# Performance work log

Hardware: AMD Instinct MI355X
Metric: run time of the kernel (lower is better)

Reference implementation:

```python
import jax, jax.numpy as jnp
import numpy as np

B, H, W, C = 16, 192, 192, 128   # batch, height, width, d_inner
R = 16      # lora_rank (bottleneck width between lora_down and lora_up)
RK = 8      # internal LoRA rank = lora_rank // 2
NC = 5      # cache_size
SCALE = 1.0 / RK        # alpha / rank with alpha = 1.0
THRESH = 0.7            # similarity_threshold
EPS = 1e-8              # torch cosine_similarity eps


def _lora_paths(x, A1, B1, A2, B2):
    # lora_down: C -> RK -> R, lora_up: R -> RK -> C, each scaled by 1/RK (dropout off in eval)
    down = ((x @ A1) @ B1) * SCALE          # [B,H,W,R]
    up = ((down @ A2) @ B2) * SCALE         # [B,H,W,C]
    return down, up


def setup_inputs() -> dict:
    key = jax.random.key(0)
    ks = jax.random.split(key, 9)
    x = jax.random.normal(ks[0], (B, H, W, C), dtype=jnp.float32)
    A1 = (jax.random.normal(ks[1], (C, RK)) / np.sqrt(C)).astype(jnp.float32)
    B1 = (jax.random.normal(ks[2], (RK, R)) / np.sqrt(RK)).astype(jnp.float32)
    A2 = (jax.random.normal(ks[3], (R, RK)) / np.sqrt(R)).astype(jnp.float32)
    B2 = (jax.random.normal(ks[4], (RK, C)) / np.sqrt(RK)).astype(jnp.float32)
    W1 = (jax.random.normal(ks[5], (C + R, C)) / np.sqrt(C + R)).astype(jnp.float32)
    b1 = jnp.zeros((C,), dtype=jnp.float32)
    W2 = (jax.random.normal(ks[6], (C, C)) / np.sqrt(C)).astype(jnp.float32)
    b2 = jnp.zeros((C,), dtype=jnp.float32)
    cache_w = jnp.array(0.5, dtype=jnp.float32)
    # Build cache entries as noisy copies of x_lora[:NC] so the first NC batch
    # elements clear the 0.7 cosine threshold (fused branch) and the rest do not.
    _, xl = _lora_paths(x, A1, B1, A2, B2)
    noise = jax.random.normal(ks[7], (NC, H, W, C), dtype=jnp.float32) * (0.05 * jnp.std(xl))
    cache_feats = xl[:NC] + noise           # [NC,H,W,C]
    return {"x": x, "A1": A1, "B1": B1, "A2": A2, "B2": B2,
            "W1": W1, "b1": b1, "W2": W2, "b2": b2,
            "cache_w": cache_w, "cache_feats": cache_feats}


def reference(x, A1, B1, A2, B2, W1, b1, W2, b2, cache_w, cache_feats):
    down, x_lora = _lora_paths(x, A1, B1, A2, B2)   # [B,H,W,R], [B,H,W,C]
    # Per-channel cosine similarity over the HW axis, averaged over channels
    num = jnp.einsum('bhwc,nhwc->bnc', x_lora, cache_feats)        # [B,NC,C]
    xn = jnp.sqrt(jnp.sum(x_lora * x_lora, axis=(1, 2)))           # [B,C]
    cn = jnp.sqrt(jnp.sum(cache_feats * cache_feats, axis=(1, 2))) # [NC,C]
    denom = jnp.maximum(xn[:, None, :], EPS) * jnp.maximum(cn[None, :, :], EPS)
    sims = jnp.mean(num / denom, axis=-1)                          # [B,NC]
    best_idx = jnp.argmax(sims, axis=1)                            # first max, like list.index
    best_sim = jnp.max(sims, axis=1)
    best = cache_feats[best_idx]                                   # [B,H,W,C]
    # Gated blend with cached feature, then fusion MLP on concat([blend, lora_down])
    cw = jax.nn.sigmoid(cache_w)
    blend = cw * x_lora + (1.0 - cw) * best
    h = jnp.concatenate([blend, down], axis=-1) @ W1 + b1          # [B,H,W,C]
    fused = jax.nn.silu(h) @ W2 + b2
    mask = (best_sim > THRESH)[:, None, None, None]
    return jnp.where(mask, fused, x_lora)
```

## Files before the change

kernel.cpp:

```cpp
#include <hip/hip_runtime.h>
#include <math.h>

#define BATCH 16
#define HWPIX 36864
#define CCH 128
#define NCACHE 5
#define SCALE 0.125f
#define THRESH 0.7f
#define EPSV 1e-8f

typedef _Float16 f16;
typedef __attribute__((ext_vector_type(8))) _Float16 f16x8;
typedef __attribute__((ext_vector_type(4))) float f32x4;

__global__ __launch_bounds__(256) void kpre1(
    const float* __restrict__ A1, const float* __restrict__ B1,
    const float* __restrict__ A2, const float* __restrict__ B2,
    const float* __restrict__ W1, const float* __restrict__ W2,
    const float* __restrict__ cache_w,
    float* __restrict__ M1f, float* __restrict__ M12f,
    f16* __restrict__ M12h, f16* __restrict__ Qh, f16* __restrict__ W2h) {
  __shared__ float M1s[128 * 16];
  __shared__ float M2s[16 * 128];
  int t = threadIdx.x;
  for (int idx = t; idx < 2048; idx += 256) {
    int i = idx >> 4, r = idx & 15;
    float s = 0.f;
    for (int k = 0; k < 8; ++k) s += A1[i * 8 + k] * B1[k * 16 + r];
    s *= SCALE;
    M1s[idx] = s;
    M1f[idx] = s;
  }
  for (int idx = t; idx < 2048; idx += 256) {
    int r = idx >> 7, j = idx & 127;
    float s = 0.f;
    for (int k = 0; k < 8; ++k) s += A2[r * 8 + k] * B2[k * 128 + j];
    M2s[idx] = s * SCALE;
  }
  __syncthreads();
  for (int idx = t; idx < 16384; idx += 256) {
    int i = idx >> 7, j = idx & 127;
    float s = 0.f;
    for (int r = 0; r < 16; ++r) s += M1s[i * 16 + r] * M2s[r * 128 + j];
    M12f[idx] = s;
    M12h[(((i >> 3) * 128 + j) << 3) + (i & 7)] = (f16)s;
  }
  float cw = 1.f / (1.f + __expf(-cache_w[0]));
  float qs = 1.f - cw;
  for (int idx = t; idx < 16384; idx += 256) {
    int k = idx >> 7, n = idx & 127;
    int ci = (((k >> 3) * 128 + n) << 3) + (k & 7);
    Qh[ci] = (f16)(qs * W1[k * 128 + n]);
    W2h[ci] = (f16)W2[k * 128 + n];
  }
}

__global__ __launch_bounds__(256) void kpre2(
    const float* __restrict__ W1, const float* __restrict__ M1f,
    const float* __restrict__ M12f, const float* __restrict__ cache_w,
    f16* __restrict__ Ph) {
  int t = threadIdx.x;
  int k = blockIdx.x * 8 + (t >> 5);
  int n0 = (t & 31) * 4;
  float cw = 1.f / (1.f + __expf(-cache_w[0]));
  float sa[4] = {0, 0, 0, 0}, sb[4] = {0, 0, 0, 0};
  for (int tt = 0; tt < 128; ++tt) {
    float m = M12f[k * 128 + tt];
    const float* wr = &W1[tt * 128 + n0];
    sa[0] += m * wr[0]; sa[1] += m * wr[1]; sa[2] += m * wr[2]; sa[3] += m * wr[3];
  }
  for (int r = 0; r < 16; ++r) {
    float m = M1f[k * 16 + r];
    const float* wr = &W1[(128 + r) * 128 + n0];
    sb[0] += m * wr[0]; sb[1] += m * wr[1]; sb[2] += m * wr[2]; sb[3] += m * wr[3];
  }
  for (int u = 0; u < 4; ++u) {
    int n = n0 + u;
    Ph[(((k >> 3) * 128 + n) << 3) + (k & 7)] = (f16)(cw * sa[u] + sb[u]);
  }
}

__global__ __launch_bounds__(256) void k2(
    const float* __restrict__ x, const float* __restrict__ cache,
    const f16* __restrict__ M12h, float* __restrict__ out,
    float* __restrict__ num, float* __restrict__ xn2, float* __restrict__ cn2) {
  __shared__ f16 Bs[16 * 128 * 8];
  __shared__ f16 As[16 * 64 * 8];
  __shared__ f16 XLb[64 * 132];
  __shared__ float nacc[2][5][128];
  __shared__ float x2acc[2][128];
  int t = threadIdx.x;
  int chunk = blockIdx.x;
  int grp = blockIdx.y;
  long pb = (long)chunk * 64;
  {
    const uint4* src = (const uint4*)M12h;
    uint4* dst = (uint4*)Bs;
    for (int i = t; i < 2048; i += 256) dst[i] = src[i];
  }
  int lane = t & 63, w = t >> 6, l15 = lane & 15, q = lane >> 4;
  for (int g = 0; g < 8; ++g) {
    int b = grp * 8 + g;
    const float* xb = x + ((long)b * HWPIX + pb) * CCH;
    __syncthreads();
    for (int i = 0; i < 8; ++i) {
      int f = i * 256 + t;
      int p = f >> 5, c4 = (f & 31) << 2;
      float4 v = ((const float4*)xb)[f];
      f16* d = &As[(((c4 >> 3) * 64 + p) << 3) + (c4 & 7)];
      d[0] = (f16)v.x; d[1] = (f16)v.y; d[2] = (f16)v.z; d[3] = (f16)v.w;
    }
    __syncthreads();
    f32x4 acc[8];
    for (int ni = 0; ni < 8; ++ni) acc[ni] = 0;
    for (int kk = 0; kk < 4; ++kk) {
      f16x8 a = *(const f16x8*)&As[(((kk * 4 + q) * 64 + (w * 16 + l15)) << 3)];
      for (int ni = 0; ni < 8; ++ni) {
        f16x8 bb = *(const f16x8*)&Bs[(((kk * 4 + q) * 128 + ni * 16 + l15)) << 3];
        acc[ni] = __builtin_amdgcn_mfma_f32_16x16x32_f16(a, bb, acc[ni], 0, 0, 0);
      }
    }
    float* ob = out + ((long)b * HWPIX + pb) * CCH;
    for (int ni = 0; ni < 8; ++ni) {
      int c = ni * 16 + l15;
      for (int r = 0; r < 4; ++r) {
        int p = w * 16 + q * 4 + r;
        float v = acc[ni][r];
        ob[(long)p * CCH + c] = v;
        XLb[p * 132 + c] = (f16)v;
      }
    }
    __syncthreads();
    {
      int c = t & 127, half = t >> 7;
      bool docn = (grp == 0) && (g == 0);
      float s2 = 0, sn0 = 0, sn1 = 0, sn2 = 0, sn3 = 0, sn4 = 0;
      float sc0 = 0, sc1 = 0, sc2 = 0, sc3 = 0, sc4 = 0;
      const float* cb = cache + pb * CCH + c;
      for (int pp = 0; pp < 32; ++pp) {
        int p = half * 32 + pp;
        float xl = (float)XLb[p * 132 + c];
        s2 += xl * xl;
        float cv0 = cb[((long)0 * HWPIX + p) * CCH];
        float cv1 = cb[((long)1 * HWPIX + p) * CCH];
        float cv2 = cb[((long)2 * HWPIX + p) * CCH];
        float cv3 = cb[((long)3 * HWPIX + p) * CCH];
        float cv4 = cb[((long)4 * HWPIX + p) * CCH];
        sn0 += xl * cv0; sn1 += xl * cv1; sn2 += xl * cv2;
        sn3 += xl * cv3; sn4 += xl * cv4;
        if (docn) {
          sc0 += cv0 * cv0; sc1 += cv1 * cv1; sc2 += cv2 * cv2;
          sc3 += cv3 * cv3; sc4 += cv4 * cv4;
        }
      }
      nacc[half][0][c] = sn0; nacc[half][1][c] = sn1; nacc[half][2][c] = sn2;
      nacc[half][3][c] = sn3; nacc[half][4][c] = sn4;
      x2acc[half][c] = s2;
      if (docn) {
        atomicAdd(&cn2[0 * 128 + c], sc0);
        atomicAdd(&cn2[1 * 128 + c], sc1);
        atomicAdd(&cn2[2 * 128 + c], sc2);
        atomicAdd(&cn2[3 * 128 + c], sc3);
        atomicAdd(&cn2[4 * 128 + c], sc4);
      }
    }
    __syncthreads();
    for (int idx = t; idx < 640; idx += 256) {
      int n = idx >> 7, cc = idx & 127;
      atomicAdd(&num[((long)b * 5 + n) * 128 + cc],
                nacc[0][n][cc] + nacc[1][n][cc]);
    }
    if (t < 128) atomicAdd(&xn2[b * 128 + t], x2acc[0][t] + x2acc[1][t]);
  }
}

__global__ __launch_bounds__(128) void k3(
    const float* __restrict__ num, const float* __restrict__ xn2v,
    const float* __restrict__ cn2v, int* __restrict__ stats) {
  __shared__ float sims[16][5];
  int t = threadIdx.x;
  if (t < 80) {
    int b = t / 5, n = t % 5;
    float s = 0.f;
    for (int c = 0; c < 128; ++c) {
      float xn = sqrtf(xn2v[b * 128 + c]);
      float cn = sqrtf(cn2v[n * 128 + c]);
      s += num[(b * 5 + n) * 128 + c] / (fmaxf(xn, EPSV) * fmaxf(cn, EPSV));
    }
    sims[b][n] = s * (1.f / 128.f);
  }
  __syncthreads();
  if (t < 16) {
    float bv = -1e30f;
    int bi = 0;
    for (int n = 0; n < 5; ++n) {
      float v = sims[t][n];
      if (v > bv) { bv = v; bi = n; }
    }
    stats[t] = bi;
    stats[16 + t] = (bv > THRESH) ? 1 : 0;
  }
}

__global__ __launch_bounds__(256) void k4(
    const float* __restrict__ x, const float* __restrict__ cache,
    const f16* __restrict__ Ph, const f16* __restrict__ Qh,
    const f16* __restrict__ W2h, const float* __restrict__ b1,
    const float* __restrict__ b2, const int* __restrict__ stats,
    float* __restrict__ out) {
  int b = blockIdx.y;
  if (!stats[16 + b]) return;
  __shared__ f16 Bs[16 * 128 * 8];
  __shared__ f16 As[16 * 64 * 8];
  __shared__ float b1s[128], b2s[128];
  int t = threadIdx.x;
  if (t < 128) { b1s[t] = b1[t]; b2s[t] = b2[t]; }
  int bi = stats[b];
  long pb = (long)blockIdx.x * 64;
  const float* xb = x + ((long)b * HWPIX + pb) * CCH;
  const float* cbest = cache + ((long)bi * HWPIX + pb) * CCH;
  int lane = t & 63, w = t >> 6, l15 = lane & 15, q = lane >> 4;

  auto stageA = [&](const float* __restrict__ src) {
    for (int i = 0; i < 8; ++i) {
      int f = i * 256 + t;
      int p = f >> 5, c4 = (f & 31) << 2;
      float4 v = ((const float4*)src)[f];
      f16* d = &As[(((c4 >> 3) * 64 + p) << 3) + (c4 & 7)];
      d[0] = (f16)v.x; d[1] = (f16)v.y; d[2] = (f16)v.z; d[3] = (f16)v.w;
    }
  };
  auto loadB = [&](const f16* __restrict__ src) {
    const uint4* s = (const uint4*)src;
    uint4* d = (uint4*)Bs;
    for (int i = t; i < 2048; i += 256) d[i] = s[i];
  };
  auto gemm = [&](f32x4* ac) {
    for (int kk = 0; kk < 4; ++kk) {
      f16x8 a = *(const f16x8*)&As[(((kk * 4 + q) * 64 + (w * 16 + l15)) << 3)];
      for (int ni = 0; ni < 8; ++ni) {
        f16x8 bb = *(const f16x8*)&Bs[(((kk * 4 + q) * 128 + ni * 16 + l15)) << 3];
        ac[ni] = __builtin_amdgcn_mfma_f32_16x16x32_f16(a, bb, ac[ni], 0, 0, 0);
      }
    }
  };

  f32x4 acc[8];
  for (int ni = 0; ni < 8; ++ni) acc[ni] = 0;
  loadB(Ph);
  stageA(xb);
  __syncthreads();
  gemm(acc);
  __syncthreads();
  loadB(Qh);
  stageA(cbest);
  __syncthreads();
  gemm(acc);
  for (int ni = 0; ni < 8; ++ni) {
    int c = ni * 16 + l15;
    for (int r = 0; r < 4; ++r) {
      int p = w * 16 + q * 4 + r;
      float hv = acc[ni][r] + b1s[c];
      float sv = hv / (1.f + __expf(-hv));
      As[(((c >> 3) * 64 + p) << 3) + (c & 7)] = (f16)sv;
    }
  }
  __syncthreads();
  loadB(W2h);
  __syncthreads();
  f32x4 acc2[8];
  for (int ni = 0; ni < 8; ++ni) acc2[ni] = 0;
  gemm(acc2);
  float* ob = out + ((long)b * HWPIX + pb) * CCH;
  for (int ni = 0; ni < 8; ++ni) {
    int c = ni * 16 + l15;
    for (int r = 0; r < 4; ++r) {
      int p = w * 16 + q * 4 + r;
      ob[(long)p * CCH + c] = acc2[ni][r] + b2s[c];
    }
  }
}

extern "C" void kernel_launch(void* const* d_in, const int* in_sizes, int n_in,
                              void* d_out, int out_size, void* d_ws, size_t ws_size,
                              hipStream_t stream) {
  const float* x  = (const float*)d_in[0];
  const float* A1 = (const float*)d_in[1];
  const float* B1 = (const float*)d_in[2];
  const float* A2 = (const float*)d_in[3];
  const float* B2 = (const float*)d_in[4];
  const float* W1 = (const float*)d_in[5];
  const float* b1 = (const float*)d_in[6];
  const float* W2 = (const float*)d_in[7];
  const float* b2 = (const float*)d_in[8];
  const float* cache_w = (const float*)d_in[9];
  const float* cache   = (const float*)d_in[10];
  float* out = (float*)d_out;
  char* wsb = (char*)d_ws;
  float* num  = (float*)(wsb + 0);
  float* xn2  = (float*)(wsb + 40960);
  float* cn2  = (float*)(wsb + 49152);
  int*   stats= (int*)  (wsb + 51712);
  float* M1f  = (float*)(wsb + 51840);
  float* M12f = (float*)(wsb + 60032);
  f16*   M12h = (f16*)  (wsb + 125568);
  f16*   Ph   = (f16*)  (wsb + 158336);
  f16*   Qh   = (f16*)  (wsb + 191104);
  f16*   W2h  = (f16*)  (wsb + 223872);

  hipMemsetAsync(wsb, 0, 51712, stream);
  kpre1<<<1, 256, 0, stream>>>(A1, B1, A2, B2, W1, W2, cache_w, M1f, M12f, M12h, Qh, W2h);
  kpre2<<<16, 256, 0, stream>>>(W1, M1f, M12f, cache_w, Ph);
  k2<<<dim3(576, 2), 256, 0, stream>>>(x, cache, M12h, out, num, xn2, cn2);
  k3<<<1, 128, 0, stream>>>(num, xn2, cn2, stats);
  k4<<<dim3(576, 16), 256, 0, stream>>>(x, cache, Ph, Qh, W2h, b1, b2, stats, out);
}
```

Before: 838.3 us.

## Load MFMA operands directly from global, vectorize reductions, widen grids

```diff
diff --git a/kernel.cpp b/kernel.cpp
--- a/kernel.cpp
+++ b/kernel.cpp
@@ -12,6 +12,13 @@
 typedef _Float16 f16;
 typedef __attribute__((ext_vector_type(8))) _Float16 f16x8;
 typedef __attribute__((ext_vector_type(4))) float f32x4;
+
+__device__ __forceinline__ float psum8(float v) {
+  v += __shfl_xor(v, 1);
+  v += __shfl_xor(v, 2);
+  v += __shfl_xor(v, 4);
+  return v;
+}
 
 __global__ __launch_bounds__(256) void kpre1(
     const float* __restrict__ A1, const float* __restrict__ B1,
@@ -23,13 +30,14 @@
   __shared__ float M1s[128 * 16];
   __shared__ float M2s[16 * 128];
   int t = threadIdx.x;
+  int blk = blockIdx.x;
   for (int idx = t; idx < 2048; idx += 256) {
     int i = idx >> 4, r = idx & 15;
     float s = 0.f;
     for (int k = 0; k < 8; ++k) s += A1[i * 8 + k] * B1[k * 16 + r];
     s *= SCALE;
     M1s[idx] = s;
-    M1f[idx] = s;
+    if (blk == 0) M1f[idx] = s;
   }
   for (int idx = t; idx < 2048; idx += 256) {
     int r = idx >> 7, j = idx & 127;
@@ -38,7 +46,7 @@
     M2s[idx] = s * SCALE;
   }
   __syncthreads();
-  for (int idx = t; idx < 16384; idx += 256) {
+  for (int idx = blk * 2048 + t; idx < blk * 2048 + 2048; idx += 256) {
     int i = idx >> 7, j = idx & 127;
     float s = 0.f;
     for (int r = 0; r < 16; ++r) s += M1s[i * 16 + r] * M2s[r * 128 + j];
@@ -47,7 +55,7 @@
   }
   float cw = 1.f / (1.f + __expf(-cache_w[0]));
   float qs = 1.f - cw;
-  for (int idx = t; idx < 16384; idx += 256) {
+  for (int idx = blk * 2048 + t; idx < blk * 2048 + 2048; idx += 256) {
     int k = idx >> 7, n = idx & 127;
     int ci = (((k >> 3) * 128 + n) << 3) + (k & 7);
     Qh[ci] = (f16)(qs * W1[k * 128 + n]);
@@ -80,97 +88,112 @@
   }
 }
 
-__global__ __launch_bounds__(256) void k2(
+__global__ __launch_bounds__(256, 4) void k2(
     const float* __restrict__ x, const float* __restrict__ cache,
     const f16* __restrict__ M12h, float* __restrict__ out,
     float* __restrict__ num, float* __restrict__ xn2, float* __restrict__ cn2) {
-  __shared__ f16 Bs[16 * 128 * 8];
-  __shared__ f16 As[16 * 64 * 8];
-  __shared__ f16 XLb[64 * 132];
-  __shared__ float nacc[2][5][128];
-  __shared__ float x2acc[2][128];
+  __shared__ f16 XLb[2][64 * 132];
   int t = threadIdx.x;
   int chunk = blockIdx.x;
   int grp = blockIdx.y;
   long pb = (long)chunk * 64;
-  {
-    const uint4* src = (const uint4*)M12h;
-    uint4* dst = (uint4*)Bs;
-    for (int i = t; i < 2048; i += 256) dst[i] = src[i];
-  }
   int lane = t & 63, w = t >> 6, l15 = lane & 15, q = lane >> 4;
-  for (int g = 0; g < 8; ++g) {
-    int b = grp * 8 + g;
+  int arow = w * 16 + l15;
+  const uint4* Bf = (const uint4*)M12h;
+  int part = t & 7;
+  int c0 = (t >> 3) * 4;
+
+  if (grp == 0) {
+    f32x4 sc[5];
+#pragma unroll
+    for (int n = 0; n < 5; ++n) sc[n] = 0;
+    const float* cp0 = cache + pb * CCH + c0;
+#pragma unroll
+    for (int pp = 0; pp < 8; ++pp) {
+      int p = part * 8 + pp;
+      const float* cp = cp0 + (long)p * CCH;
+#pragma unroll
+      for (int n = 0; n < 5; ++n) {
+        f32x4 cv = *(const f32x4*)(cp + (long)n * HWPIX * CCH);
+        sc[n] += cv * cv;
+      }
+    }
+#pragma unroll
+    for (int n = 0; n < 5; ++n)
+#pragma unroll
+      for (int j = 0; j < 4; ++j) {
+        float v = psum8(sc[n][j]);
+        if (part == 0) atomicAdd(&cn2[n * 128 + c0 + j], v);
+      }
+  }
+
+  for (int g = 0; g < 4; ++g) {
+    int b = grp * 4 + g;
     const float* xb = x + ((long)b * HWPIX + pb) * CCH;
-    __syncthreads();
-    for (int i = 0; i < 8; ++i) {
-      int f = i * 256 + t;
-      int p = f >> 5, c4 = (f & 31) << 2;
-      float4 v = ((const float4*)xb)[f];
-      f16* d = &As[(((c4 >> 3) * 64 + p) << 3) + (c4 & 7)];
-      d[0] = (f16)v.x; d[1] = (f16)v.y; d[2] = (f16)v.z; d[3] = (f16)v.w;
-    }
-    __syncthreads();
+    f16* xl_s = XLb[g & 1];
     f32x4 acc[8];
+#pragma unroll
     for (int ni = 0; ni < 8; ++ni) acc[ni] = 0;
+#pragma unroll
     for (int kk = 0; kk < 4; ++kk) {
-      f16x8 a = *(const f16x8*)&As[(((kk * 4 + q) * 64 + (w * 16 + l15)) << 3)];
+      const float* ap = xb + arow * CCH + kk * 32 + q * 8;
+      f32x4 a0 = *(const f32x4*)ap;
+      f32x4 a1 = *(const f32x4*)(ap + 4);
+      f16x8 a;
+      a[0] = (f16)a0[0]; a[1] = (f16)a0[1]; a[2] = (f16)a0[2]; a[3] = (f16)a0[3];
+      a[4] = (f16)a1[0]; a[5] = (f16)a1[1]; a[6] = (f16)a1[2]; a[7] = (f16)a1[3];
+#pragma unroll
       for (int ni = 0; ni < 8; ++ni) {
-        f16x8 bb = *(const f16x8*)&Bs[(((kk * 4 + q) * 128 + ni * 16 + l15)) << 3];
-        acc[ni] = __builtin_amdgcn_mfma_f32_16x16x32_f16(a, bb, acc[ni], 0, 0, 0);
+        uint4 bw = Bf[(kk * 4 + q) * 128 + ni * 16 + l15];
+        acc[ni] = __builtin_amdgcn_mfma_f32_16x16x32_f16(a, *(const f16x8*)&bw,
+                                                         acc[ni], 0, 0, 0);
       }
     }
     float* ob = out + ((long)b * HWPIX + pb) * CCH;
+#pragma unroll
     for (int ni = 0; ni < 8; ++ni) {
       int c = ni * 16 + l15;
+#pragma unroll
       for (int r = 0; r < 4; ++r) {
         int p = w * 16 + q * 4 + r;
         float v = acc[ni][r];
         ob[(long)p * CCH + c] = v;
-        XLb[p * 132 + c] = (f16)v;
+        xl_s[p * 132 + c] = (f16)v;
       }
     }
     __syncthreads();
-    {
-      int c = t & 127, half = t >> 7;
-      bool docn = (grp == 0) && (g == 0);
-      float s2 = 0, sn0 = 0, sn1 = 0, sn2 = 0, sn3 = 0, sn4 = 0;
-      float sc0 = 0, sc1 = 0, sc2 = 0, sc3 = 0, sc4 = 0;
-      const float* cb = cache + pb * CCH + c;
-      for (int pp = 0; pp < 32; ++pp) {
-        int p = half * 32 + pp;
-        float xl = (float)XLb[p * 132 + c];
-        s2 += xl * xl;
-        float cv0 = cb[((long)0 * HWPIX + p) * CCH];
-        float cv1 = cb[((long)1 * HWPIX + p) * CCH];
-        float cv2 = cb[((long)2 * HWPIX + p) * CCH];
-        float cv3 = cb[((long)3 * HWPIX + p) * CCH];
-        float cv4 = cb[((long)4 * HWPIX + p) * CCH];
-        sn0 += xl * cv0; sn1 += xl * cv1; sn2 += xl * cv2;
-        sn3 += xl * cv3; sn4 += xl * cv4;
-        if (docn) {
-          sc0 += cv0 * cv0; sc1 += cv1 * cv1; sc2 += cv2 * cv2;
-          sc3 += cv3 * cv3; sc4 += cv4 * cv4;
-        }
-      }
-      nacc[half][0][c] = sn0; nacc[half][1][c] = sn1; nacc[half][2][c] = sn2;
-      nacc[half][3][c] = sn3; nacc[half][4][c] = sn4;
-      x2acc[half][c] = s2;
-      if (docn) {
-        atomicAdd(&cn2[0 * 128 + c], sc0);
-        atomicAdd(&cn2[1 * 128 + c], sc1);
-        atomicAdd(&cn2[2 * 128 + c], sc2);
-        atomicAdd(&cn2[3 * 128 + c], sc3);
-        atomicAdd(&cn2[4 * 128 + c], sc4);
-      }
-    }
-    __syncthreads();
-    for (int idx = t; idx < 640; idx += 256) {
-      int n = idx >> 7, cc = idx & 127;
-      atomicAdd(&num[((long)b * 5 + n) * 128 + cc],
-                nacc[0][n][cc] + nacc[1][n][cc]);
-    }
-    if (t < 128) atomicAdd(&xn2[b * 128 + t], x2acc[0][t] + x2acc[1][t]);
+    f32x4 sn[5], s2;
+#pragma unroll
+    for (int n = 0; n < 5; ++n) sn[n] = 0;
+    s2 = 0;
+    const float* cq0 = cache + pb * CCH + c0;
+#pragma unroll
+    for (int pp = 0; pp < 8; ++pp) {
+      int p = part * 8 + pp;
+      const f16* xr = &xl_s[p * 132 + c0];
+      f32x4 xv;
+      xv[0] = (float)xr[0]; xv[1] = (float)xr[1];
+      xv[2] = (float)xr[2]; xv[3] = (float)xr[3];
+      const float* cp = cq0 + (long)p * CCH;
+#pragma unroll
+      for (int n = 0; n < 5; ++n) {
+        f32x4 cv = *(const f32x4*)(cp + (long)n * HWPIX * CCH);
+        sn[n] += xv * cv;
+      }
+      s2 += xv * xv;
+    }
+#pragma unroll
+    for (int n = 0; n < 5; ++n)
+#pragma unroll
+      for (int j = 0; j < 4; ++j) {
+        float v = psum8(sn[n][j]);
+        if (part == 0) atomicAdd(&num[((long)b * 5 + n) * 128 + c0 + j], v);
+      }
+#pragma unroll
+    for (int j = 0; j < 4; ++j) {
+      float v = psum8(s2[j]);
+      if (part == 0) atomicAdd(&xn2[b * 128 + c0 + j], v);
+    }
   }
 }
 
@@ -202,7 +225,7 @@
   }
 }
 
-__global__ __launch_bounds__(256) void k4(
+__global__ __launch_bounds__(256, 4) void k4(
     const float* __restrict__ x, const float* __restrict__ cache,
     const f16* __restrict__ Ph, const f16* __restrict__ Qh,
     const f16* __restrict__ W2h, const float* __restrict__ b1,
@@ -210,73 +233,84 @@
     float* __restrict__ out) {
   int b = blockIdx.y;
   if (!stats[16 + b]) return;
-  __shared__ f16 Bs[16 * 128 * 8];
   __shared__ f16 As[16 * 64 * 8];
-  __shared__ float b1s[128], b2s[128];
-  int t = threadIdx.x;
-  if (t < 128) { b1s[t] = b1[t]; b2s[t] = b2[t]; }
+  int t = threadIdx.x;
   int bi = stats[b];
   long pb = (long)blockIdx.x * 64;
   const float* xb = x + ((long)b * HWPIX + pb) * CCH;
-  const float* cbest = cache + ((long)bi * HWPIX + pb) * CCH;
+  const float* cb = cache + ((long)bi * HWPIX + pb) * CCH;
   int lane = t & 63, w = t >> 6, l15 = lane & 15, q = lane >> 4;
-
-  auto stageA = [&](const float* __restrict__ src) {
-    for (int i = 0; i < 8; ++i) {
-      int f = i * 256 + t;
-      int p = f >> 5, c4 = (f & 31) << 2;
-      float4 v = ((const float4*)src)[f];
-      f16* d = &As[(((c4 >> 3) * 64 + p) << 3) + (c4 & 7)];
-      d[0] = (f16)v.x; d[1] = (f16)v.y; d[2] = (f16)v.z; d[3] = (f16)v.w;
-    }
-  };
-  auto loadB = [&](const f16* __restrict__ src) {
-    const uint4* s = (const uint4*)src;
-    uint4* d = (uint4*)Bs;
-    for (int i = t; i < 2048; i += 256) d[i] = s[i];
-  };
-  auto gemm = [&](f32x4* ac) {
-    for (int kk = 0; kk < 4; ++kk) {
-      f16x8 a = *(const f16x8*)&As[(((kk * 4 + q) * 64 + (w * 16 + l15)) << 3)];
-      for (int ni = 0; ni < 8; ++ni) {
-        f16x8 bb = *(const f16x8*)&Bs[(((kk * 4 + q) * 128 + ni * 16 + l15)) << 3];
-        ac[ni] = __builtin_amdgcn_mfma_f32_16x16x32_f16(a, bb, ac[ni], 0, 0, 0);
-      }
-    }
-  };
+  int arow = w * 16 + l15;
+  const uint4* Pf = (const uint4*)Ph;
+  const uint4* Qf = (const uint4*)Qh;
+  const uint4* Wf = (const uint4*)W2h;
 
   f32x4 acc[8];
+#pragma unroll
   for (int ni = 0; ni < 8; ++ni) acc[ni] = 0;
-  loadB(Ph);
-  stageA(xb);
-  __syncthreads();
-  gemm(acc);
-  __syncthreads();
-  loadB(Qh);
-  stageA(cbest);
-  __syncthreads();
-  gemm(acc);
+#pragma unroll
+  for (int kk = 0; kk < 4; ++kk) {
+    const float* ap = xb + arow * CCH + kk * 32 + q * 8;
+    f32x4 a0 = *(const f32x4*)ap;
+    f32x4 a1 = *(const f32x4*)(ap + 4);
+    f16x8 a;
+    a[0] = (f16)a0[0]; a[1] = (f16)a0[1]; a[2] = (f16)a0[2]; a[3] = (f16)a0[3];
+    a[4] = (f16)a1[0]; a[5] = (f16)a1[1]; a[6] = (f16)a1[2]; a[7] = (f16)a1[3];
+#pragma unroll
+    for (int ni = 0; ni < 8; ++ni) {
+      uint4 bw = Pf[(kk * 4 + q) * 128 + ni * 16 + l15];
+      acc[ni] = __builtin_amdgcn_mfma_f32_16x16x32_f16(a, *(const f16x8*)&bw,
+                                                       acc[ni], 0, 0, 0);
+    }
+  }
+#pragma unroll
+  for (int kk = 0; kk < 4; ++kk) {
+    const float* ap = cb + arow * CCH + kk * 32 + q * 8;
+    f32x4 a0 = *(const f32x4*)ap;
+    f32x4 a1 = *(const f32x4*)(ap + 4);
+    f16x8 a;
+    a[0] = (f16)a0[0]; a[1] = (f16)a0[1]; a[2] = (f16)a0[2]; a[3] = (f16)a0[3];
+    a[4] = (f16)a1[0]; a[5] = (f16)a1[1]; a[6] = (f16)a1[2]; a[7] = (f16)a1[3];
+#pragma unroll
+    for (int ni = 0; ni < 8; ++ni) {
+      uint4 bw = Qf[(kk * 4 + q) * 128 + ni * 16 + l15];
+      acc[ni] = __builtin_amdgcn_mfma_f32_16x16x32_f16(a, *(const f16x8*)&bw,
+                                                       acc[ni], 0, 0, 0);
+    }
+  }
+#pragma unroll
   for (int ni = 0; ni < 8; ++ni) {
     int c = ni * 16 + l15;
+    float b1v = b1[c];
+#pragma unroll
     for (int r = 0; r < 4; ++r) {
       int p = w * 16 + q * 4 + r;
-      float hv = acc[ni][r] + b1s[c];
+      float hv = acc[ni][r] + b1v;
       float sv = hv / (1.f + __expf(-hv));
       As[(((c >> 3) * 64 + p) << 3) + (c & 7)] = (f16)sv;
     }
   }
-  __syncthreads();
-  loadB(W2h);
-  __syncthreads();
-  f32x4 acc2[8];
-  for (int ni = 0; ni < 8; ++ni) acc2[ni] = 0;
-  gemm(acc2);
+#pragma unroll
+  for (int ni = 0; ni < 8; ++ni) acc[ni] = 0;
+#pragma unroll
+  for (int kk = 0; kk < 4; ++kk) {
+    f16x8 a = *(const f16x8*)&As[((kk * 4 + q) * 64 + arow) << 3];
+#pragma unroll
+    for (int ni = 0; ni < 8; ++ni) {
+      uint4 bw = Wf[(kk * 4 + q) * 128 + ni * 16 + l15];
+      acc[ni] = __builtin_amdgcn_mfma_f32_16x16x32_f16(a, *(const f16x8*)&bw,
+                                                       acc[ni], 0, 0, 0);
+    }
+  }
   float* ob = out + ((long)b * HWPIX + pb) * CCH;
+#pragma unroll
   for (int ni = 0; ni < 8; ++ni) {
     int c = ni * 16 + l15;
+    float b2v = b2[c];
+#pragma unroll
     for (int r = 0; r < 4; ++r) {
       int p = w * 16 + q * 4 + r;
-      ob[(long)p * CCH + c] = acc2[ni][r] + b2s[c];
+      ob[(long)p * CCH + c] = acc[ni][r] + b2v;
     }
   }
 }
@@ -309,9 +343,9 @@
   f16*   W2h  = (f16*)  (wsb + 223872);
 
   hipMemsetAsync(wsb, 0, 51712, stream);
-  kpre1<<<1, 256, 0, stream>>>(A1, B1, A2, B2, W1, W2, cache_w, M1f, M12f, M12h, Qh, W2h);
+  kpre1<<<8, 256, 0, stream>>>(A1, B1, A2, B2, W1, W2, cache_w, M1f, M12f, M12h, Qh, W2h);
   kpre2<<<16, 256, 0, stream>>>(W1, M1f, M12f, cache_w, Ph);
-  k2<<<dim3(576, 2), 256, 0, stream>>>(x, cache, M12h, out, num, xn2, cn2);
+  k2<<<dim3(576, 4), 256, 0, stream>>>(x, cache, M12h, out, num, xn2, cn2);
   k3<<<1, 128, 0, stream>>>(num, xn2, cn2, stats);
   k4<<<dim3(576, 16), 256, 0, stream>>>(x, cache, Ph, Qh, W2h, b1, b2, stats, out);
 }
```

Result: slower. 1.579 ms (+88.3%).
